# Optimization experiments

Measured on AMD Instinct MI355X. Metric: run time of the kernel, lower is better.

The kernel has to match this reference:

```python
import jax, jax.numpy as jnp
import numpy as np

TOP_K = 4
N_GROUP = 4
TOPK_GROUP = 2
ROUTED_SCALE = 2.5


def grouped_matmul(x, w, group_sizes):
    """x: [N, k] rows sorted by expert; w: [E, k, n]; group_sizes: [E] int32."""
    if hasattr(jax.lax, "ragged_dot"):
        return jax.lax.ragged_dot(x, w, group_sizes)
    # Fallback: expert id per row via searchsorted on cumulative counts, masked dense GEMMs.
    eid = jnp.searchsorted(jnp.cumsum(group_sizes), jnp.arange(x.shape[0]), side="right")
    out = jnp.zeros((x.shape[0], w.shape[-1]), x.dtype)
    for e in range(w.shape[0]):
        out = out + jnp.where((eid == e)[:, None], x @ w[e], 0.0)
    return out


def setup_inputs() -> dict:
    key = jax.random.key(0)
    ks = jax.random.split(key, 9)
    b, s, h, i, E = 2, 2048, 1024, 512, 32
    return {
        "hidden_states": jax.random.normal(ks[0], (b, s, h), jnp.float32),
        "gate_weight": jax.random.normal(ks[1], (E, h), jnp.float32) * 0.02,
        "expert_bias": jnp.zeros((E,), jnp.float32),
        "w_gate": jax.random.normal(ks[2], (E, h, i), jnp.float32) * 0.02,
        "w_up": jax.random.normal(ks[3], (E, h, i), jnp.float32) * 0.02,
        "w_down": jax.random.normal(ks[4], (E, i, h), jnp.float32) * 0.02,
        "ws_gate": jax.random.normal(ks[5], (h, i), jnp.float32) * 0.02,
        "ws_up": jax.random.normal(ks[6], (h, i), jnp.float32) * 0.02,
        "ws_down": jax.random.normal(ks[7], (i, h), jnp.float32) * 0.02,
    }


def reference(hidden_states, gate_weight, expert_bias, w_gate, w_up, w_down,
              ws_gate, ws_up, ws_down):
    b, s, h = hidden_states.shape
    E = gate_weight.shape[0]
    x = hidden_states.reshape(-1, h)          # [T, h]
    T = x.shape[0]

    # --- gate (LLaDA2MoeGate) ---
    logits = x.astype(jnp.float32) @ gate_weight.T.astype(jnp.float32)  # [T, E]
    scores = jax.nn.sigmoid(logits)
    s_rt = scores + expert_bias
    # group-limited top-k: score each group by sum of its top-2 experts
    grp = s_rt.reshape(T, N_GROUP, E // N_GROUP)
    grp_score = jax.lax.top_k(grp, 2)[0].sum(-1)                         # [T, G]
    _, gidx = jax.lax.top_k(grp_score, TOPK_GROUP)
    gmask = jnp.zeros((T, N_GROUP), jnp.float32).at[jnp.arange(T)[:, None], gidx].set(1.0)
    smask = jnp.repeat(gmask, E // N_GROUP, axis=1)                      # [T, E]
    masked = jnp.where(smask > 0, s_rt, -jnp.inf)
    _, topk_idx = jax.lax.top_k(masked, TOP_K)                           # [T, K]
    tw = jnp.take_along_axis(scores, topk_idx, axis=1)
    tw = tw / (tw.sum(-1, keepdims=True) + 1e-20) * ROUTED_SCALE         # [T, K]

    # --- moe_infer: sort by expert, grouped GEMMs, unsort + weighted combine ---
    flat = topk_idx.reshape(-1)                                          # [T*K]
    order = jnp.argsort(flat)
    xs = x[order // TOP_K]                                               # [N, h] sorted by expert
    counts = jnp.bincount(flat, length=E).astype(jnp.int32)
    g = grouped_matmul(xs, w_gate, counts)
    u = grouped_matmul(xs, w_up, counts)
    out_s = grouped_matmul(jax.nn.silu(g) * u, w_down, counts)           # [N, h]
    y = jnp.zeros_like(out_s).at[order].set(out_s)                       # unsort
    y = (y.reshape(T, TOP_K, h) * tw[:, :, None]).sum(1)

    # --- shared experts (SwiGLU MLP on identity) ---
    shared = (jax.nn.silu(x @ ws_gate) * (x @ ws_up)) @ ws_down
    y = (y + shared).reshape(b, s, h)
    return y, logits.reshape(b, s, E), topk_idx.reshape(b, s, TOP_K)
```

## Files before the change

### kernel.cpp

```cpp
#include <hip/hip_runtime.h>
#include <stdint.h>

typedef __attribute__((ext_vector_type(8))) short short8;
typedef __attribute__((ext_vector_type(4))) float f32x4;

#define NR_ROUTED 16384
#define NROWS     20480
#define MAXTILES  192

__device__ __forceinline__ float bf2f(unsigned short h) {
  return __uint_as_float(((unsigned)h) << 16);
}
__device__ __forceinline__ unsigned short f2bf(float f) {
  unsigned u = __float_as_uint(f);
  u = (u + 0x7FFFu + ((u >> 16) & 1u)) >> 16;
  return (unsigned short)u;
}

__global__ void tcast_kernel(const float* __restrict__ src0, const float* __restrict__ src1,
                             unsigned short* __restrict__ dst, int Kd, int Nd,
                             int n_mul, int n_add) {
  __shared__ float tl[64][65];
  int tilesK = Kd >> 6;
  int tk = blockIdx.x % tilesK, tn = blockIdx.x / tilesK;
  int e = blockIdx.y;
  const float* src = (e < 32) ? (src0 + (size_t)e * Kd * Nd) : src1;
  int k0 = tk * 64, n0 = tn * 64;
  int tid = threadIdx.x;
#pragma unroll
  for (int p = 0; p < 4; ++p) {
    int f = p * 256 + tid;
    int r = f >> 4, c4 = (f & 15) * 4;
    float4 v = *(const float4*)(src + (size_t)(k0 + r) * Nd + n0 + c4);
    tl[c4 + 0][r] = v.x; tl[c4 + 1][r] = v.y; tl[c4 + 2][r] = v.z; tl[c4 + 3][r] = v.w;
  }
  __syncthreads();
#pragma unroll
  for (int p = 0; p < 4; ++p) {
    int f = p * 256 + tid;
    int n = f >> 4, kc = (f & 15) * 4;
    ushort4 o;
    o.x = f2bf(tl[n][kc + 0]); o.y = f2bf(tl[n][kc + 1]);
    o.z = f2bf(tl[n][kc + 2]); o.w = f2bf(tl[n][kc + 3]);
    *(ushort4*)(dst + ((size_t)e * 1024 + (size_t)(n0 + n) * n_mul + n_add) * Kd + k0 + kc) = o;
  }
}

__global__ void gwt_kernel(const float* __restrict__ gw, float* __restrict__ gwt) {
  int idx = blockIdx.x * 256 + threadIdx.x;
  int e = idx & 31, j4 = idx >> 5;
  float4 v = *(const float4*)(gw + (size_t)e * 1024 + j4 * 4);
  *(float4*)(gwt + ((size_t)j4 * 32 + e) * 4) = v;
}

__global__ __launch_bounds__(256) void routing_kernel(
    const float* __restrict__ x, const float* __restrict__ gwt,
    const float* __restrict__ bias, unsigned short* __restrict__ xb,
    float* __restrict__ logits_out, float* __restrict__ topk_f,
    int* __restrict__ topk_i, float* __restrict__ tw,
    int* __restrict__ counts) {
  int tid = threadIdx.x;
  int tbase = blockIdx.x * 8;
  const float4* xsrc = (const float4*)(x + (size_t)tbase * 1024);
  ushort4* xbd = (ushort4*)(xb + (size_t)tbase * 1024);
#pragma unroll
  for (int p = 0; p < 8; ++p) {
    float4 v = xsrc[p * 256 + tid];
    ushort4 o;
    o.x = f2bf(v.x); o.y = f2bf(v.y); o.z = f2bf(v.z); o.w = f2bf(v.w);
    xbd[p * 256 + tid] = o;
  }
  int lane = tid & 63, w = tid >> 6;
  int tok2 = lane >> 5, e = lane & 31, h = lane & 32;
  int t = tbase + w * 2 + tok2;
  const float* xrow = x + (size_t)t * 1024;
  float acc = 0.f;
#pragma unroll 8
  for (int j = 0; j < 256; ++j) {
    float4 xv = *(const float4*)(xrow + j * 4);
    float4 wv = *(const float4*)(gwt + ((size_t)j * 32 + e) * 4);
    acc += xv.x * wv.x + xv.y * wv.y + xv.z * wv.z + xv.w * wv.w;
  }
  logits_out[(size_t)t * 32 + e] = acc;
  float sg = 1.f / (1.f + expf(-acc));
  float srt = sg + bias[e];
  float m1 = srt, m2 = -1e30f;
#pragma unroll
  for (int off = 1; off < 8; off <<= 1) {
    float o1 = __shfl_xor(m1, off);
    float o2 = __shfl_xor(m2, off);
    if (o1 > m1) { m2 = fmaxf(m1, o2); m1 = o1; }
    else         { m2 = fmaxf(m2, o1); }
  }
  float gsv = m1 + m2;
  float q0 = __shfl(gsv, h + 0), q1 = __shfl(gsv, h + 8);
  float q2 = __shfl(gsv, h + 16), q3 = __shfl(gsv, h + 24);
  int ga = 0; float bv = q0;
  if (q1 > bv) { ga = 1; bv = q1; }
  if (q2 > bv) { ga = 2; bv = q2; }
  if (q3 > bv) { ga = 3; bv = q3; }
  int gb = -1; float bw = -1e30f;
  if (ga != 0) { gb = 0; bw = q0; }
  if (ga != 1 && q1 > bw) { gb = 1; bw = q1; }
  if (ga != 2 && q2 > bw) { gb = 2; bw = q2; }
  if (ga != 3 && q3 > bw) { gb = 3; bw = q3; }
  unsigned allowed = (0xFFu << (ga * 8)) | (0xFFu << (gb * 8));
  unsigned u = __float_as_uint(srt);
  u = (u & 0x80000000u) ? ~u : (u | 0x80000000u);
  unsigned long long key = ((unsigned long long)u << 32) | (unsigned)(31 - e);
  if (!((allowed >> e) & 1u)) key = 0ull;
  unsigned packed = 0;
  float wsum = 0.f;
#pragma unroll
  for (int k = 0; k < 4; ++k) {
    unsigned long long kk = key;
#pragma unroll
    for (int off = 1; off < 32; off <<= 1) {
      unsigned long long o = __shfl_xor(kk, off);
      if (o > kk) kk = o;
    }
    int ek = 31 - (int)(kk & 0xFFFFFFFFull);
    float sge = __shfl(sg, h + ek);
    wsum += sge;
    packed |= (unsigned)ek << (8 * k);
    if (e == ek) key = 0ull;
  }
  float scale = 2.5f / (wsum + 1e-20f);
  int kq = e & 3;
  int myek = (int)((packed >> (8 * kq)) & 0xFFu);
  float mysg = __shfl(sg, h + myek);
  if (e < 4) {
    int t4 = t * 4 + e;
    topk_i[t4] = myek;
    topk_f[t4] = (float)myek;
    tw[t4] = mysg * scale;
    atomicAdd(&counts[myek], 1);
  }
}

__global__ void build_tiles_kernel(const int* __restrict__ counts, int* __restrict__ cursor,
                                   int4* __restrict__ table, int* __restrict__ n_tiles) {
  if (threadIdx.x != 0) return;
  int base = 0, nt = 0;
  for (int e = 0; e < 32; ++e) {
    cursor[e] = base;
    int n = counts[e];
    for (int j = 0; j < n; j += 128) {
      int rem = n - j;
      table[nt] = make_int4(e, base + j, rem < 128 ? rem : 128, 0);
      ++nt;
    }
    base += n;
  }
  for (int j = 0; j < 32; ++j) {
    table[nt] = make_int4(32, NR_ROUTED + j * 128, 128, 0);
    ++nt;
  }
  *n_tiles = nt;
}

__global__ void assign_kernel(const int* __restrict__ topk_i, int* __restrict__ cursor,
                              int* __restrict__ perm, int* __restrict__ pos) {
  int idx = blockIdx.x * 256 + threadIdx.x;
  if (idx < NR_ROUTED) {
    int e = topk_i[idx];
    int p = atomicAdd(&cursor[e], 1);
    perm[p] = idx >> 2;
    pos[idx] = p;
  } else {
    perm[idx] = idx - NR_ROUTED;
  }
}

__global__ __launch_bounds__(256, 2) void gemm_kernel(
    const unsigned short* __restrict__ A, const unsigned short* __restrict__ B,
    unsigned short* __restrict__ C, const int* __restrict__ perm,
    const int4* __restrict__ table, const int* __restrict__ n_tiles,
    int K, int use_perm, int fuse_silu, int out_stride) {
  __shared__ unsigned short Al[2 * 128 * 64];
  __shared__ unsigned short Bl[2 * 128 * 64];
  if ((int)blockIdx.x >= *n_tiles) return;
  int4 te = table[blockIdx.x];
  int eidx = te.x, row_start = te.y, nrows = te.z;
  int n0 = blockIdx.y * 128;
  int tid = threadIdx.x, lane = tid & 63, wave = tid >> 6;
  int wr = wave >> 1, wc = wave & 1;

  const unsigned short* aBase[4];
  const unsigned short* bBase[4];
  int lOff[4];
#pragma unroll
  for (int i = 0; i < 4; ++i) {
    int s = wave * 64 + i * 256 + lane;
    int row = s >> 3, cseg = s & 7;
    int rowg = row_start + row;
    int tok = use_perm ? perm[rowg] : rowg;
    aBase[i] = A + (size_t)tok * K + cseg * 8;
    bBase[i] = B + (size_t)eidx * 1024 * K + (size_t)(n0 + row) * K + cseg * 8;
    lOff[i] = (wave * 64 + i * 256) * 8;
  }
  f32x4 acc[4][4];
  f32x4 z = {0.f, 0.f, 0.f, 0.f};
#pragma unroll
  for (int a = 0; a < 4; ++a)
#pragma unroll
    for (int b = 0; b < 4; ++b) acc[a][b] = z;

  int nsteps = K >> 6;
#pragma unroll
  for (int i = 0; i < 4; ++i) {
    __builtin_amdgcn_global_load_lds(
        (const __attribute__((address_space(1))) unsigned int*)(aBase[i]),
        (__attribute__((address_space(3))) unsigned int*)&Al[lOff[i]], 16, 0, 0);
    __builtin_amdgcn_global_load_lds(
        (const __attribute__((address_space(1))) unsigned int*)(bBase[i]),
        (__attribute__((address_space(3))) unsigned int*)&Bl[lOff[i]], 16, 0, 0);
  }
  for (int s = 0; s < nsteps; ++s) {
    int cur = s & 1;
    const unsigned short* Ac = &Al[cur * (128 * 64)];
    const unsigned short* Bc = &Bl[cur * (128 * 64)];
    asm volatile("s_waitcnt vmcnt(0)" ::: "memory");
    __syncthreads();
    if (s + 1 < nsteps) {
      int ko = (s + 1) << 6;
      unsigned short* An = &Al[(cur ^ 1) * (128 * 64)];
      unsigned short* Bn = &Bl[(cur ^ 1) * (128 * 64)];
#pragma unroll
      for (int i = 0; i < 4; ++i) {
        __builtin_amdgcn_global_load_lds(
            (const __attribute__((address_space(1))) unsigned int*)(aBase[i] + ko),
            (__attribute__((address_space(3))) unsigned int*)&An[lOff[i]], 16, 0, 0);
        __builtin_amdgcn_global_load_lds(
            (const __attribute__((address_space(1))) unsigned int*)(bBase[i] + ko),
            (__attribute__((address_space(3))) unsigned int*)&Bn[lOff[i]], 16, 0, 0);
      }
    }
#pragma unroll
    for (int ks = 0; ks < 2; ++ks) {
      short8 af[4], bfr[4];
#pragma unroll
      for (int rf = 0; rf < 4; ++rf) {
        int m = wr * 64 + rf * 16 + (lane & 15);
        af[rf] = *(const short8*)&Ac[m * 64 + ks * 32 + (lane >> 4) * 8];
      }
#pragma unroll
      for (int cf = 0; cf < 4; ++cf) {
        int n = wc * 64 + cf * 16 + (lane & 15);
        bfr[cf] = *(const short8*)&Bc[n * 64 + ks * 32 + (lane >> 4) * 8];
      }
#pragma unroll
      for (int rf = 0; rf < 4; ++rf)
#pragma unroll
        for (int cf = 0; cf < 4; ++cf)
          acc[rf][cf] = __builtin_amdgcn_mfma_f32_16x16x32_bf16(af[rf], bfr[cf], acc[rf][cf], 0, 0, 0);
    }
  }
  int q = lane >> 4, cl = lane & 15;
  if (fuse_silu) {
    bool even = (cl & 1) == 0;
#pragma unroll
    for (int rf = 0; rf < 4; ++rf) {
#pragma unroll
      for (int r = 0; r < 4; ++r) {
        int rowl = wr * 64 + rf * 16 + q * 4 + r;
        size_t rowg = (size_t)(row_start + rowl);
#pragma unroll
        for (int cf = 0; cf < 4; ++cf) {
          float v = acc[rf][cf][r];
          float other = __shfl_xor(v, 1);
          if (even && rowl < nrows) {
            float g = v, u = other;
            float a = g / (1.f + expf(-g)) * u;
            int pcol = (n0 >> 1) + wc * 32 + cf * 8 + (cl >> 1);
            C[rowg * out_stride + pcol] = f2bf(a);
          }
        }
      }
    }
  } else {
#pragma unroll
    for (int rf = 0; rf < 4; ++rf) {
#pragma unroll
      for (int r = 0; r < 4; ++r) {
        int rowl = wr * 64 + rf * 16 + q * 4 + r;
        if (rowl < nrows) {
          size_t rowg = (size_t)(row_start + rowl);
#pragma unroll
          for (int cf = 0; cf < 4; ++cf) {
            int colg = n0 + wc * 64 + cf * 16 + cl;
            C[rowg * out_stride + colg] = f2bf(acc[rf][cf][r]);
          }
        }
      }
    }
  }
}

__global__ void combine_kernel(const unsigned short* __restrict__ outs,
                               const int* __restrict__ pos, const float* __restrict__ tw,
                               float* __restrict__ y) {
  int t = blockIdx.x, tid = threadIdx.x;
  int c = tid * 4;
  ushort4 sv = *(const ushort4*)(outs + (size_t)(NR_ROUTED + t) * 1024 + c);
  float y0 = bf2f(sv.x), y1 = bf2f(sv.y), y2 = bf2f(sv.z), y3 = bf2f(sv.w);
#pragma unroll
  for (int k = 0; k < 4; ++k) {
    int p = pos[t * 4 + k];
    float w = tw[t * 4 + k];
    ushort4 v = *(const ushort4*)(outs + (size_t)p * 1024 + c);
    y0 += w * bf2f(v.x); y1 += w * bf2f(v.y); y2 += w * bf2f(v.z); y3 += w * bf2f(v.w);
  }
  float4 o = {y0, y1, y2, y3};
  *(float4*)(y + (size_t)t * 1024 + c) = o;
}

extern "C" void kernel_launch(void* const* d_in, const int* in_sizes, int n_in,
                              void* d_out, int out_size, void* d_ws, size_t ws_size,
                              hipStream_t stream) {
  const float* x       = (const float*)d_in[0];
  const float* gw      = (const float*)d_in[1];
  const float* bias    = (const float*)d_in[2];
  const float* w_gate  = (const float*)d_in[3];
  const float* w_up    = (const float*)d_in[4];
  const float* w_down  = (const float*)d_in[5];
  const float* ws_gate = (const float*)d_in[6];
  const float* ws_up   = (const float*)d_in[7];
  const float* ws_down = (const float*)d_in[8];

  char* ws = (char*)d_ws;
  size_t off = 0;
  auto alloc = [&](size_t bytes) {
    void* p = ws + off;
    off = (off + bytes + 255) & ~(size_t)255;
    return p;
  };
  unsigned short* wgu = (unsigned short*)alloc(33ull * 1024 * 1024 * 2);
  unsigned short* wd  = (unsigned short*)alloc(33ull * 1024 * 512 * 2);
  unsigned short* xb  = (unsigned short*)alloc(4096ull * 1024 * 2);
  unsigned short* gu  = (unsigned short*)alloc((size_t)NROWS * 1024 * 2);
  unsigned short* act = (unsigned short*)alloc((size_t)NROWS * 512 * 2);
  float* gwt    = (float*)alloc(32 * 1024 * 4);
  int*   counts = (int*)alloc(32 * 4);
  int*   cursor = (int*)alloc(32 * 4);
  int*   ntiles = (int*)alloc(256);
  int4*  table  = (int4*)alloc(256 * 16);
  int*   perm   = (int*)alloc(NROWS * 4);
  int*   topk_i = (int*)alloc(NR_ROUTED * 4);
  int*   pos    = (int*)alloc(NR_ROUTED * 4);
  float* tw     = (float*)alloc(NR_ROUTED * 4);
  (void)ws_size; (void)in_sizes; (void)n_in; (void)out_size;

  float* out_y      = (float*)d_out;
  float* out_logits = out_y + 4096ull * 1024;
  float* out_topk   = out_logits + 4096ull * 32;

  hipMemsetAsync(counts, 0, 32 * 4, stream);
  gwt_kernel<<<32, 256, 0, stream>>>(gw, gwt);
  tcast_kernel<<<dim3(128, 33), 256, 0, stream>>>(w_gate, ws_gate, wgu, 1024, 512, 2, 0);
  tcast_kernel<<<dim3(128, 33), 256, 0, stream>>>(w_up,   ws_up,   wgu, 1024, 512, 2, 1);
  tcast_kernel<<<dim3(128, 33), 256, 0, stream>>>(w_down, ws_down, wd,  512, 1024, 1, 0);
  routing_kernel<<<512, 256, 0, stream>>>(x, gwt, bias, xb, out_logits, out_topk, topk_i, tw, counts);
  build_tiles_kernel<<<1, 64, 0, stream>>>(counts, cursor, table, ntiles);
  assign_kernel<<<80, 256, 0, stream>>>(topk_i, cursor, perm, pos);
  gemm_kernel<<<dim3(MAXTILES, 8), 256, 0, stream>>>(xb, wgu, act, perm, table, ntiles, 1024, 1, 1, 512);
  gemm_kernel<<<dim3(MAXTILES, 8), 256, 0, stream>>>(act, wd, gu, perm, table, ntiles, 512, 0, 0, 1024);
  combine_kernel<<<4096, 256, 0, stream>>>(gu, pos, tw, out_y);
}
```

Measured before the change: 512.4 us.

## Swizzle GEMM LDS layout, single-buffer tiles, swap grid axes, parallel tile table build

The GEMM now stores LDS tiles with an XOR swizzle on 16-byte column chunks, so the MFMA fragment reads avoid bank conflicts. It also drops LDS double buffering for a single buffer with load, wait, compute and sync each K step, which halves LDS use and may allow more resident blocks but removes load/compute overlap. The grid is transposed so N-column blocks of the same row tile launch next to each other, which should improve L2 reuse of the gathered A rows. The tile table build switches from a single serial thread to a wave-level prefix scan.

```diff
diff --git a/kernel.cpp b/kernel.cpp
--- a/kernel.cpp
+++ b/kernel.cpp
@@ -140,23 +140,33 @@
 
 __global__ void build_tiles_kernel(const int* __restrict__ counts, int* __restrict__ cursor,
                                    int4* __restrict__ table, int* __restrict__ n_tiles) {
-  if (threadIdx.x != 0) return;
-  int base = 0, nt = 0;
-  for (int e = 0; e < 32; ++e) {
-    cursor[e] = base;
-    int n = counts[e];
-    for (int j = 0; j < n; j += 128) {
-      int rem = n - j;
-      table[nt] = make_int4(e, base + j, rem < 128 ? rem : 128, 0);
-      ++nt;
-    }
-    base += n;
-  }
-  for (int j = 0; j < 32; ++j) {
-    table[nt] = make_int4(32, NR_ROUTED + j * 128, 128, 0);
-    ++nt;
-  }
-  *n_tiles = nt;
+  int lane = threadIdx.x;
+  int c = (lane < 32) ? counts[lane] : 0;
+  int incl = c;
+#pragma unroll
+  for (int off = 1; off < 32; off <<= 1) {
+    int v = __shfl_up(incl, off);
+    if (lane >= off) incl += v;
+  }
+  int base = incl - c;
+  int nt_e = (c + 127) >> 7;
+  int tincl = nt_e;
+#pragma unroll
+  for (int off = 1; off < 32; off <<= 1) {
+    int v = __shfl_up(tincl, off);
+    if (lane >= off) tincl += v;
+  }
+  int toff = tincl - nt_e;
+  int tot = __shfl(tincl, 31);
+  if (lane < 32) {
+    cursor[lane] = base;
+    for (int j = 0; j < nt_e; ++j) {
+      int rem = c - j * 128;
+      table[toff + j] = make_int4(lane, base + j * 128, rem < 128 ? rem : 128, 0);
+    }
+    table[tot + lane] = make_int4(32, NR_ROUTED + lane * 128, 128, 0);
+  }
+  if (lane == 0) *n_tiles = tot + 32;
 }
 
 __global__ void assign_kernel(const int* __restrict__ topk_i, int* __restrict__ cursor,
@@ -177,12 +187,12 @@
     unsigned short* __restrict__ C, const int* __restrict__ perm,
     const int4* __restrict__ table, const int* __restrict__ n_tiles,
     int K, int use_perm, int fuse_silu, int out_stride) {
-  __shared__ unsigned short Al[2 * 128 * 64];
-  __shared__ unsigned short Bl[2 * 128 * 64];
-  if ((int)blockIdx.x >= *n_tiles) return;
-  int4 te = table[blockIdx.x];
+  __shared__ unsigned short Al[128 * 64];
+  __shared__ unsigned short Bl[128 * 64];
+  if ((int)blockIdx.y >= *n_tiles) return;
+  int4 te = table[blockIdx.y];
   int eidx = te.x, row_start = te.y, nrows = te.z;
-  int n0 = blockIdx.y * 128;
+  int n0 = blockIdx.x * 128;
   int tid = threadIdx.x, lane = tid & 63, wave = tid >> 6;
   int wr = wave >> 1, wc = wave & 1;
 
@@ -192,12 +202,13 @@
 #pragma unroll
   for (int i = 0; i < 4; ++i) {
     int s = wave * 64 + i * 256 + lane;
-    int row = s >> 3, cseg = s & 7;
+    int row = s >> 3, c = s & 7;
+    int cd = c ^ (row & 7);
     int rowg = row_start + row;
     int tok = use_perm ? perm[rowg] : rowg;
-    aBase[i] = A + (size_t)tok * K + cseg * 8;
-    bBase[i] = B + (size_t)eidx * 1024 * K + (size_t)(n0 + row) * K + cseg * 8;
-    lOff[i] = (wave * 64 + i * 256) * 8;
+    aBase[i] = A + (size_t)tok * K + cd * 8;
+    bBase[i] = B + (size_t)eidx * 1024 * K + (size_t)(n0 + row) * K + cd * 8;
+    lOff[i] = s * 8;
   }
   f32x4 acc[4][4];
   f32x4 z = {0.f, 0.f, 0.f, 0.f};
@@ -206,48 +217,35 @@
 #pragma unroll
     for (int b = 0; b < 4; ++b) acc[a][b] = z;
 
-  int nsteps = K >> 6;
-#pragma unroll
-  for (int i = 0; i < 4; ++i) {
-    __builtin_amdgcn_global_load_lds(
-        (const __attribute__((address_space(1))) unsigned int*)(aBase[i]),
-        (__attribute__((address_space(3))) unsigned int*)&Al[lOff[i]], 16, 0, 0);
-    __builtin_amdgcn_global_load_lds(
-        (const __attribute__((address_space(1))) unsigned int*)(bBase[i]),
-        (__attribute__((address_space(3))) unsigned int*)&Bl[lOff[i]], 16, 0, 0);
-  }
-  for (int s = 0; s < nsteps; ++s) {
-    int cur = s & 1;
-    const unsigned short* Ac = &Al[cur * (128 * 64)];
-    const unsigned short* Bc = &Bl[cur * (128 * 64)];
+  int mrow = wr * 64 + (lane & 15);
+  int nrow = wc * 64 + (lane & 15);
+  int qq = lane >> 4;
+
+  for (int k0 = 0; k0 < K; k0 += 64) {
+#pragma unroll
+    for (int i = 0; i < 4; ++i) {
+      __builtin_amdgcn_global_load_lds(
+          (const __attribute__((address_space(1))) unsigned int*)(aBase[i] + k0),
+          (__attribute__((address_space(3))) unsigned int*)&Al[lOff[i]], 16, 0, 0);
+      __builtin_amdgcn_global_load_lds(
+          (const __attribute__((address_space(1))) unsigned int*)(bBase[i] + k0),
+          (__attribute__((address_space(3))) unsigned int*)&Bl[lOff[i]], 16, 0, 0);
+    }
     asm volatile("s_waitcnt vmcnt(0)" ::: "memory");
     __syncthreads();
-    if (s + 1 < nsteps) {
-      int ko = (s + 1) << 6;
-      unsigned short* An = &Al[(cur ^ 1) * (128 * 64)];
-      unsigned short* Bn = &Bl[(cur ^ 1) * (128 * 64)];
-#pragma unroll
-      for (int i = 0; i < 4; ++i) {
-        __builtin_amdgcn_global_load_lds(
-            (const __attribute__((address_space(1))) unsigned int*)(aBase[i] + ko),
-            (__attribute__((address_space(3))) unsigned int*)&An[lOff[i]], 16, 0, 0);
-        __builtin_amdgcn_global_load_lds(
-            (const __attribute__((address_space(1))) unsigned int*)(bBase[i] + ko),
-            (__attribute__((address_space(3))) unsigned int*)&Bn[lOff[i]], 16, 0, 0);
+#pragma unroll
+    for (int ks = 0; ks < 2; ++ks) {
+      int j = ks * 4 + qq;
+      short8 af[4], bfr[4];
+#pragma unroll
+      for (int rf = 0; rf < 4; ++rf) {
+        int m = mrow + rf * 16;
+        af[rf] = *(const short8*)&Al[m * 64 + (j ^ (m & 7)) * 8];
       }
-    }
-#pragma unroll
-    for (int ks = 0; ks < 2; ++ks) {
-      short8 af[4], bfr[4];
-#pragma unroll
-      for (int rf = 0; rf < 4; ++rf) {
-        int m = wr * 64 + rf * 16 + (lane & 15);
-        af[rf] = *(const short8*)&Ac[m * 64 + ks * 32 + (lane >> 4) * 8];
-      }
 #pragma unroll
       for (int cf = 0; cf < 4; ++cf) {
-        int n = wc * 64 + cf * 16 + (lane & 15);
-        bfr[cf] = *(const short8*)&Bc[n * 64 + ks * 32 + (lane >> 4) * 8];
+        int n = nrow + cf * 16;
+        bfr[cf] = *(const short8*)&Bl[n * 64 + (j ^ (n & 7)) * 8];
       }
 #pragma unroll
       for (int rf = 0; rf < 4; ++rf)
@@ -255,6 +253,7 @@
         for (int cf = 0; cf < 4; ++cf)
           acc[rf][cf] = __builtin_amdgcn_mfma_f32_16x16x32_bf16(af[rf], bfr[cf], acc[rf][cf], 0, 0, 0);
     }
+    __syncthreads();
   }
   int q = lane >> 4, cl = lane & 15;
   if (fuse_silu) {
@@ -363,7 +362,7 @@
   routing_kernel<<<512, 256, 0, stream>>>(x, gwt, bias, xb, out_logits, out_topk, topk_i, tw, counts);
   build_tiles_kernel<<<1, 64, 0, stream>>>(counts, cursor, table, ntiles);
   assign_kernel<<<80, 256, 0, stream>>>(topk_i, cursor, perm, pos);
-  gemm_kernel<<<dim3(MAXTILES, 8), 256, 0, stream>>>(xb, wgu, act, perm, table, ntiles, 1024, 1, 1, 512);
-  gemm_kernel<<<dim3(MAXTILES, 8), 256, 0, stream>>>(act, wd, gu, perm, table, ntiles, 512, 0, 0, 1024);
+  gemm_kernel<<<dim3(8, MAXTILES), 256, 0, stream>>>(xb, wgu, act, perm, table, ntiles, 1024, 1, 1, 512);
+  gemm_kernel<<<dim3(8, MAXTILES), 256, 0, stream>>>(act, wd, gu, perm, table, ntiles, 512, 0, 0, 1024);
   combine_kernel<<<4096, 256, 0, stream>>>(gu, pos, tw, out_y);
 }
```

New measurement: 463.7 us. -9.5%, faster.
